# Performance work log

Measured on AMD Instinct MI355X. Metric: run time of the kernel, lower is better.

## Reference

```python
import jax, jax.numpy as jnp
import numpy as np


def _conv(x, w, b, pad):
    y = jax.lax.conv_general_dilated(
        x, w, window_strides=(1, 1), padding=[(pad, pad), (pad, pad)],
        dimension_numbers=('NCHW', 'OIHW', 'NCHW'))
    return y + b[None, :, None, None]


def _grid_sample(img, gxn, gyn):
    # img [N,C,H,W]; gxn,gyn [N,H,W] normalized coords.
    # Matches torch grid_sample(mode='bilinear', padding_mode='zeros', align_corners=False).
    N, C, H, W = img.shape
    ix = ((gxn + 1.0) * W - 1.0) * 0.5
    iy = ((gyn + 1.0) * H - 1.0) * 0.5
    ix0 = jnp.floor(ix); iy0 = jnp.floor(iy)
    ix1 = ix0 + 1.0; iy1 = iy0 + 1.0
    wx1 = ix - ix0; wy1 = iy - iy0
    wx0 = 1.0 - wx1; wy0 = 1.0 - wy1
    bidx = jnp.arange(N)[:, None, None]

    def gather(yy, xx):
        valid = (xx >= 0) & (xx < W) & (yy >= 0) & (yy < H)
        xc = jnp.clip(xx, 0, W - 1).astype(jnp.int32)
        yc = jnp.clip(yy, 0, H - 1).astype(jnp.int32)
        v = img[bidx, :, yc, xc]  # [N,H,W,C]
        return jnp.where(valid[..., None], v, jnp.zeros((), img.dtype))

    out = (gather(iy0, ix0) * (wy0 * wx0)[..., None]
           + gather(iy0, ix1) * (wy0 * wx1)[..., None]
           + gather(iy1, ix0) * (wy1 * wx0)[..., None]
           + gather(iy1, ix1) * (wy1 * wx1)[..., None])
    return jnp.transpose(out, (0, 3, 1, 2))  # [N,C,H,W]


def reference(inputs, state, i2h_w, i2h_b, i2f_w, i2f_b, h2f_w, h2f_b,
              flows_w, flows_b, wrap_w, wrap_b):
    B, T, Cin, H, W = inputs.shape
    hid = state.shape[1]
    L = flows_w.shape[0] // 2

    # input-to-hidden for all timesteps at once (as in the torch code)
    i2h = _conv(inputs.reshape(B * T, Cin, H, W), i2h_w, i2h_b, 1)
    i2h = i2h.reshape(B, T, 3 * hid, H, W)
    r_i, u_i, n_i = jnp.split(i2h, 3, axis=2)

    gx, gy = jnp.meshgrid(jnp.arange(W, dtype=inputs.dtype),
                          jnp.arange(H, dtype=inputs.dtype))  # each [H,W]

    def step(h, xs):
        x_t, r_t, u_t, n_t = xs
        f = jnp.tanh(_conv(x_t, i2f_w, i2f_b, 2) + _conv(h, h2f_w, h2f_b, 2))
        flows = _conv(f, flows_w, flows_b, 2).reshape(B, L, 2, H, W)
        # vgrid = grid + (-flow), then normalize by 2*v/size - 1
        vx = gx[None, None] - flows[:, :, 0]
        vy = gy[None, None] - flows[:, :, 1]
        gxn = 2.0 * vx / W - 1.0
        gyn = 2.0 * vy / H - 1.0
        img = jnp.broadcast_to(h[:, None], (B, L, hid, H, W)).reshape(B * L, hid, H, W)
        warped = _grid_sample(img, gxn.reshape(B * L, H, W), gyn.reshape(B * L, H, W))
        warped = warped.reshape(B, L * hid, H, W)
        h2h = _conv(warped, wrap_w, wrap_b, 0)
        r_h, u_h, n_h = jnp.split(h2h, 3, axis=1)
        r = jax.nn.sigmoid(r_t + r_h)
        u = jax.nn.sigmoid(u_t + u_h)
        n = jax.nn.sigmoid(n_t + r * n_h)  # note: sigmoid, faithful to source
        h_new = (1.0 - u) * n + u * h
        return h_new, h_new

    xs = (jnp.swapaxes(inputs, 0, 1),
          jnp.swapaxes(r_i, 0, 1),
          jnp.swapaxes(u_i, 0, 1),
          jnp.swapaxes(n_i, 0, 1))
    h_last, outs = jax.lax.scan(step, state, xs)
    outputs = jnp.swapaxes(outs, 0, 1)  # [B,T,hid,H,W]
    return outputs, h_last


def setup_inputs() -> dict:
    key = jax.random.key(0)
    ks = jax.random.split(key, 8)
    B, T, Cin, H, W = 4, 10, 8, 96, 96
    hid, L = 64, 13

    def w(k, shape):
        fan_in = int(np.prod(shape[1:]))
        return jax.random.normal(k, shape, jnp.float32) * (1.0 / np.sqrt(fan_in))

    return {
        'inputs': jax.random.normal(ks[0], (B, T, Cin, H, W), jnp.float32),
        'state': jnp.zeros((B, hid, H, W), jnp.float32),
        'i2h_w': w(ks[1], (3 * hid, Cin, 3, 3)), 'i2h_b': jnp.zeros((3 * hid,), jnp.float32),
        'i2f_w': w(ks[2], (32, Cin, 5, 5)), 'i2f_b': jnp.zeros((32,), jnp.float32),
        'h2f_w': w(ks[3], (32, hid, 5, 5)), 'h2f_b': jnp.zeros((32,), jnp.float32),
        'flows_w': w(ks[4], (2 * L, 32, 5, 5)), 'flows_b': jnp.zeros((2 * L,), jnp.float32),
        'wrap_w': w(ks[5], (3 * hid, hid * L, 1, 1)), 'wrap_b': jnp.zeros((3 * hid,), jnp.float32),
    }
```

## Files before the change

kernel.cpp:

```cpp
#include <hip/hip_runtime.h>
#include <math.h>

#define HW 9216

typedef __attribute__((ext_vector_type(8))) short short8;
typedef __attribute__((ext_vector_type(4))) short short4v;
typedef __attribute__((ext_vector_type(4))) float float4v;

__device__ __forceinline__ float sigmoidf_(float x) { return 1.0f / (1.0f + expf(-x)); }

__device__ __forceinline__ short bf16rne(float f) {
  unsigned u = __builtin_bit_cast(unsigned, f);
  unsigned r = (u + 0x7FFFu + ((u >> 16) & 1u)) >> 16;
  return (short)r;
}
__device__ __forceinline__ float bf2f(short s) {
  return __builtin_bit_cast(float, ((unsigned)(unsigned short)s) << 16);
}

__global__ __launch_bounds__(256) void k_wconv(const float* __restrict__ w,
                                               short* __restrict__ o)
{
  int i = blockIdx.x * 256 + threadIdx.x;
  if (i >= 192 * 832) return;
  int n = i / 832, k = i % 832;
  int l = k >> 6, c = k & 63;
  o[((size_t)l * 192 + n) * 64 + c] = bf16rne(w[i]);
}

__global__ __launch_bounds__(256) void k_pack(
    const float* __restrict__ wh, const float* __restrict__ wi,
    const float* __restrict__ flw, const float* __restrict__ wih,
    short* __restrict__ whK, short* __restrict__ wiK, short* __restrict__ flK,
    short* __restrict__ i2hK)
{
  int i = blockIdx.x * 256 + threadIdx.x;
  if (i < 51200) {
    int t = i / 2048, rem = i % 2048;
    int o = rem / 64, c = rem % 64;
    whK[i] = bf16rne(wh[((size_t)(o * 64 + c)) * 25 + t]);
  } else if (i < 58368) {
    int j = i - 51200;
    int g = j / 1024, rem = j % 1024;
    int o = rem / 32, k = rem % 32;
    int q = k / 8, ch = k % 8;
    int tap = g * 4 + q;
    wiK[j] = (tap < 25) ? bf16rne(wi[((size_t)(o * 8 + ch)) * 25 + tap]) : (short)0;
  } else if (i < 83968) {
    int j = i - 58368;
    int t = j / 1024, rem = j % 1024;
    int o = rem / 32, c = rem % 32;
    flK[j] = (o < 26) ? bf16rne(flw[((size_t)(o * 32 + c)) * 25 + t]) : (short)0;
  } else {
    int j = i - 83968;
    int g = j / 6144, rem = j % 6144;
    int n = rem / 32, k = rem % 32;
    int q = k / 8, ch = k % 8;
    int tap = g * 4 + q;
    i2hK[j] = (tap < 9) ? bf16rne(wih[((size_t)(n * 8 + ch)) * 9 + tap]) : (short)0;
  }
}

__global__ __launch_bounds__(256) void k_h2bf(const float* __restrict__ st,
                                              short* __restrict__ hbf)
{
  const int tid = threadIdx.x;
  const int pp = tid & 63, cg = tid >> 6;
  const int b = blockIdx.y;
  const int p = blockIdx.x * 64 + pp;
  short s[16];
  #pragma unroll
  for (int k = 0; k < 16; ++k)
    s[k] = bf16rne(st[((size_t)b * 64 + cg * 16 + k) * HW + p]);
  short* dst = hbf + ((size_t)b * HW + p) * 64 + cg * 16;
  *(short8*)dst = *(short8*)&s[0];
  *(short8*)(dst + 8) = *(short8*)&s[8];
}

__global__ __launch_bounds__(256) void k_x2bf(const float* __restrict__ inp,
                                              short* __restrict__ xbf)
{
  const int p  = blockIdx.x * 256 + threadIdx.x;
  const int bt = blockIdx.y;
  short s[8];
  #pragma unroll
  for (int ci = 0; ci < 8; ++ci)
    s[ci] = bf16rne(inp[((size_t)bt * 8 + ci) * HW + p]);
  *(short8*)(xbf + ((size_t)bt * HW + p) * 8) = *(short8*)s;
}

__global__ __launch_bounds__(256) void k_i2h(
    const short* __restrict__ xbf, int t_off,
    const short* __restrict__ wK, const float* __restrict__ bias,
    short* __restrict__ out)
{
  __shared__ __align__(16) short lds_o[192 * 136];
  const int tid  = threadIdx.x;
  const int lane = tid & 63;
  const int w    = tid >> 6;
  const int ml = lane & 15, qd = lane >> 4;
  const int zz = blockIdx.y;
  const int t = (zz >> 2) + t_off, b = zz & 3;
  const int pw0 = blockIdx.x * 128 + w * 32;
  const short* xb = xbf + ((size_t)(b * 10 + t)) * HW * 8;

  short8 afr[2][3];
  #pragma unroll
  for (int s = 0; s < 2; ++s) {
    int px0 = pw0 + s * 16;
    int y0 = px0 / 96, xc0 = px0 % 96;
    #pragma unroll
    for (int g = 0; g < 3; ++g) {
      int tap = g * 4 + qd;
      int dy = tap / 3 - 1;
      int dx = tap % 3 - 1;
      int yy = y0 + dy, xx = xc0 + ml + dx;
      bool v = (tap < 9) && (yy >= 0) && (yy < 96) && (xx >= 0) && (xx < 96);
      short8 a = {};
      if (v) a = *(const short8*)(xb + (size_t)(px0 + ml + dy * 96 + dx) * 8);
      afr[s][g] = a;
    }
  }

  float4v acc[2][12];
  #pragma unroll
  for (int s = 0; s < 2; ++s)
    #pragma unroll
    for (int j = 0; j < 12; ++j)
      #pragma unroll
      for (int r = 0; r < 4; ++r) acc[s][j][r] = 0.0f;

  #pragma unroll
  for (int j = 0; j < 12; ++j) {
    #pragma unroll
    for (int g = 0; g < 3; ++g) {
      short8 bf = *(const short8*)(wK + ((size_t)(g * 192 + j * 16 + ml)) * 32 + qd * 8);
      acc[0][j] = __builtin_amdgcn_mfma_f32_16x16x32_bf16(afr[0][g], bf, acc[0][j], 0, 0, 0);
      acc[1][j] = __builtin_amdgcn_mfma_f32_16x16x32_bf16(afr[1][g], bf, acc[1][j], 0, 0, 0);
    }
  }

  #pragma unroll
  for (int j = 0; j < 12; ++j) {
    float bv = bias[j * 16 + ml];
    #pragma unroll
    for (int s = 0; s < 2; ++s) {
      short4v o4;
      #pragma unroll
      for (int r = 0; r < 4; ++r) o4[r] = bf16rne(acc[s][j][r] + bv);
      *(short4v*)(lds_o + (j * 16 + ml) * 136 + w * 32 + s * 16 + qd * 4) = o4;
    }
  }
  __syncthreads();
  const int pblk = blockIdx.x * 128;
  #pragma unroll
  for (int k = 0; k < 12; ++k) {
    int r = (tid >> 4) + k * 16;
    short8 vvv = *(short8*)(lds_o + r * 136 + (tid & 15) * 8);
    *(short8*)(out + ((size_t)(zz * 192 + r)) * HW + pblk + (tid & 15) * 8) = vvv;
  }
}

__global__ __launch_bounds__(256) void k_f(
    const short* __restrict__ xbf, int t,
    const short* __restrict__ hbf,
    const short* __restrict__ whK,
    const short* __restrict__ wiK,
    const float* __restrict__ bi, const float* __restrict__ bh,
    short* __restrict__ fbf)
{
  const int tid = threadIdx.x;
  const int lane = tid & 63;
  const int w = tid >> 6;
  const int ml = lane & 15, qd = lane >> 4;
  const int b = blockIdx.y;
  const int px0 = blockIdx.x * 64 + w * 16;
  const int y0 = px0 / 96, xc0 = px0 % 96;
  const int xcol = xc0 + ml;
  const int px = px0 + ml;
  const short* hb = hbf + (size_t)b * HW * 64;
  const short* xb = xbf + ((size_t)(b * 10 + t)) * HW * 8;

  float4v acc0 = {0.f, 0.f, 0.f, 0.f};
  float4v acc1 = {0.f, 0.f, 0.f, 0.f};

  #pragma unroll
  for (int ky = 0; ky < 5; ++ky) {
    int yy = y0 + ky - 2;
    if (yy < 0 || yy >= 96) continue;
    #pragma unroll
    for (int kx = 0; kx < 5; ++kx) {
      int xx = xcol + kx - 2;
      bool cv = (xx >= 0) && (xx < 96);
      int off = (ky - 2) * 96 + (kx - 2);
      const short* ap = hb + (size_t)(px + off) * 64 + qd * 8;
      short8 a0 = {}, a1 = {};
      if (cv) { a0 = *(const short8*)ap; a1 = *(const short8*)(ap + 32); }
      int tap = ky * 5 + kx;
      const short* bp = whK + ((size_t)tap * 32 + ml) * 64 + qd * 8;
      short8 b00 = *(const short8*)bp;
      short8 b01 = *(const short8*)(bp + 32);
      short8 b10 = *(const short8*)(bp + 16 * 64);
      short8 b11 = *(const short8*)(bp + 16 * 64 + 32);
      acc0 = __builtin_amdgcn_mfma_f32_16x16x32_bf16(a0, b00, acc0, 0, 0, 0);
      acc0 = __builtin_amdgcn_mfma_f32_16x16x32_bf16(a1, b01, acc0, 0, 0, 0);
      acc1 = __builtin_amdgcn_mfma_f32_16x16x32_bf16(a0, b10, acc1, 0, 0, 0);
      acc1 = __builtin_amdgcn_mfma_f32_16x16x32_bf16(a1, b11, acc1, 0, 0, 0);
    }
  }

  #pragma unroll
  for (int g = 0; g < 7; ++g) {
    int tap = g * 4 + qd;
    int dy = tap / 5 - 2;
    int dx = tap - (dy + 2) * 5 - 2;
    int yy = y0 + dy, xx = xcol + dx;
    bool v = (tap < 25) && (yy >= 0) && (yy < 96) && (xx >= 0) && (xx < 96);
    short8 a = {};
    if (v) a = *(const short8*)(xb + (size_t)(px + dy * 96 + dx) * 8);
    const short* bp = wiK + ((size_t)g * 32 + ml) * 32 + qd * 8;
    short8 b0 = *(const short8*)bp;
    short8 b1 = *(const short8*)(bp + 16 * 32);
    acc0 = __builtin_amdgcn_mfma_f32_16x16x32_bf16(a, b0, acc0, 0, 0, 0);
    acc1 = __builtin_amdgcn_mfma_f32_16x16x32_bf16(a, b1, acc1, 0, 0, 0);
  }

  short* fo = fbf + (size_t)b * HW * 32;
  #pragma unroll
  for (int i = 0; i < 2; ++i) {
    int o = i * 16 + ml;
    float bias = bi[o] + bh[o];
    float4v a = i ? acc1 : acc0;
    #pragma unroll
    for (int r = 0; r < 4; ++r) {
      int p2 = px0 + qd * 4 + r;
      fo[(size_t)p2 * 32 + o] = bf16rne(tanhf(a[r] + bias));
    }
  }
}

__global__ __launch_bounds__(256) void k_flows(
    const short* __restrict__ fbf,
    const short* __restrict__ flK,
    const float* __restrict__ bias,
    float* __restrict__ fls)
{
  const int tid = threadIdx.x;
  const int lane = tid & 63;
  const int w = tid >> 6;
  const int ml = lane & 15, qd = lane >> 4;
  const int b = blockIdx.y;
  const int px0 = blockIdx.x * 64 + w * 16;
  const int y0 = px0 / 96, xc0 = px0 % 96;
  const int xcol = xc0 + ml;
  const int px = px0 + ml;
  const short* fb = fbf + (size_t)b * HW * 32;

  float4v acc0 = {0.f, 0.f, 0.f, 0.f};
  float4v acc1 = {0.f, 0.f, 0.f, 0.f};

  #pragma unroll
  for (int ky = 0; ky < 5; ++ky) {
    int yy = y0 + ky - 2;
    if (yy < 0 || yy >= 96) continue;
    #pragma unroll
    for (int kx = 0; kx < 5; ++kx) {
      int xx = xcol + kx - 2;
      bool cv = (xx >= 0) && (xx < 96);
      int off = (ky - 2) * 96 + (kx - 2);
      short8 a = {};
      if (cv) a = *(const short8*)(fb + (size_t)(px + off) * 32 + qd * 8);
      int tap = ky * 5 + kx;
      const short* bp = flK + ((size_t)tap * 32 + ml) * 32 + qd * 8;
      short8 b0 = *(const short8*)bp;
      short8 b1 = *(const short8*)(bp + 16 * 32);
      acc0 = __builtin_amdgcn_mfma_f32_16x16x32_bf16(a, b0, acc0, 0, 0, 0);
      acc1 = __builtin_amdgcn_mfma_f32_16x16x32_bf16(a, b1, acc1, 0, 0, 0);
    }
  }

  float* fo = fls + (size_t)b * 26 * HW;
  #pragma unroll
  for (int i = 0; i < 2; ++i) {
    int o = i * 16 + ml;
    if (o < 26) {
      float bv = bias[o];
      float4v a = i ? acc1 : acc0;
      #pragma unroll
      for (int r = 0; r < 4; ++r)
        fo[(size_t)o * HW + px0 + qd * 4 + r] = a[r] + bv;
    }
  }
}

__global__ __launch_bounds__(256, 3) void k_fused(
    const float* __restrict__ fls,
    const float* __restrict__ hbase, long long hstr,
    const short* __restrict__ hbf_in,
    const short* __restrict__ i2h,
    const short* __restrict__ wbf,
    const float* __restrict__ wb,
    float* __restrict__ outb, long long ostr,
    short* __restrict__ hbf_out,
    float* __restrict__ lastb)
{
  __shared__ __align__(16) char smem_raw[50176];
  short* lds_v0 = (short*)smem_raw;
  short* lds_v1 = lds_v0 + 64 * 80;
  float* lds_f  = (float*)(smem_raw + 20480);
  float* lds_h  = (float*)smem_raw;
  short* hpack  = (short*)smem_raw;

  const int tid = threadIdx.x;
  const int pp  = tid & 63;
  const int cg  = tid >> 6;
  const int ii  = blockIdx.x;
  const int xcd = ii & 7;
  const int b   = xcd >> 1;
  const int tile = ((ii >> 3) << 1) | (xcd & 1);
  const int p   = tile * 64 + pp;
  const int ypix = p / 96, xpix = p % 96;
  const float* hb  = hbase + (size_t)b * hstr;
  const short* hvp = hbf_in + ((size_t)b * HW) * 64 + cg * 16;
  const float* flb = fls + (size_t)b * 26 * HW;
  const int ml = pp & 15;
  const int qd = pp >> 4;
  const short* wfb = wbf + ((size_t)(48 * cg + ml)) * 64 + qd * 8;

  #pragma unroll
  for (int it = 0; it < 7; ++it) {
    int idx = it * 256 + tid;
    if (idx < 1664) {
      int c = idx >> 6, pp2 = idx & 63;
      lds_f[pp2 * 26 + c] = flb[(size_t)c * HW + tile * 64 + pp2];
    }
  }

  float4v acc[3][4];
  #pragma unroll
  for (int i = 0; i < 3; ++i)
    #pragma unroll
    for (int j = 0; j < 4; ++j)
      #pragma unroll
      for (int r = 0; r < 4; ++r) acc[i][j][r] = 0.0f;

  int   o_[4];
  float wt_[4];
  short8 u_[4][2];
  short8 wp[3][2];
  short vv[16];

  auto comp_offs = [&](int l) {
    float fx = lds_f[pp * 26 + 2 * l];
    float fy = lds_f[pp * 26 + 2 * l + 1];
    float ix = (float)xpix - fx - 0.5f;
    float iy = (float)ypix - fy - 0.5f;
    float x0f = floorf(ix), y0f = floorf(iy);
    float wx1 = ix - x0f, wy1 = iy - y0f;
    float wx0 = 1.0f - wx1, wy0 = 1.0f - wy1;
    int x0 = (int)x0f, y0 = (int)y0f;
    bool vx0 = (x0 >= 0) && (x0 < 96);
    bool vx1 = (x0 + 1 >= 0) && (x0 + 1 < 96);
    bool vy0g = (y0 >= 0) && (y0 < 96);
    bool vy1g = (y0 + 1 >= 0) && (y0 + 1 < 96);
    o_[0] = (vx0 && vy0g) ? (y0 * 96 + x0)           : -1;
    o_[1] = (vx1 && vy0g) ? (y0 * 96 + x0 + 1)       : -1;
    o_[2] = (vx0 && vy1g) ? ((y0 + 1) * 96 + x0)     : -1;
    o_[3] = (vx1 && vy1g) ? ((y0 + 1) * 96 + x0 + 1) : -1;
    wt_[0] = wy0 * wx0; wt_[1] = wy0 * wx1; wt_[2] = wy1 * wx0; wt_[3] = wy1 * wx1;
  };
  auto load_gather = [&]() {
    #pragma unroll
    for (int q = 0; q < 4; ++q) {
      short8 z = {};
      u_[q][0] = z; u_[q][1] = z;
      if (o_[q] >= 0) {
        const short* tp = hvp + (size_t)o_[q] * 64;
        u_[q][0] = *(const short8*)tp;
        u_[q][1] = *(const short8*)(tp + 8);
      }
    }
  };
  auto load_w = [&](int l) {
    const short* wsrc = wfb + (size_t)l * 192 * 64;
    #pragma unroll
    for (int i = 0; i < 3; ++i) {
      wp[i][0] = *(const short8*)(wsrc + (i * 16) * 64);
      wp[i][1] = *(const short8*)(wsrc + (i * 16) * 64 + 32);
    }
  };
  auto comp_vv = [&]() {
    float sum[16];
    #pragma unroll
    for (int k = 0; k < 16; ++k) sum[k] = 0.0f;
    #pragma unroll
    for (int q = 0; q < 4; ++q) {
      #pragma unroll
      for (int k = 0; k < 8; ++k) {
        sum[k]     += wt_[q] * bf2f(u_[q][0][k]);
        sum[k + 8] += wt_[q] * bf2f(u_[q][1][k]);
      }
    }
    #pragma unroll
    for (int k = 0; k < 16; ++k) vv[k] = bf16rne(sum[k]);
  };
  auto store_vv = [&](short* buf) {
    *(short8*)(buf + pp * 80 + cg * 16)     = *(short8*)&vv[0];
    *(short8*)(buf + pp * 80 + cg * 16 + 8) = *(short8*)&vv[8];
  };

  __syncthreads();
  comp_offs(0);
  load_gather();
  load_w(0);
  comp_vv();
  store_vv(lds_v0);

  for (int l = 0; l < 13; ++l) {
    __syncthreads();
    if (l < 12) {
      comp_offs(l + 1);
      load_gather();
    }
    short* rbuf = (l & 1) ? lds_v1 : lds_v0;
    #pragma unroll
    for (int ks = 0; ks < 2; ++ks) {
      short8 bfr[4];
      #pragma unroll
      for (int j = 0; j < 4; ++j)
        bfr[j] = *(const short8*)(rbuf + (j * 16 + ml) * 80 + ks * 32 + qd * 8);
      #pragma unroll
      for (int i = 0; i < 3; ++i)
        #pragma unroll
        for (int j = 0; j < 4; ++j)
          acc[i][j] = __builtin_amdgcn_mfma_f32_16x16x32_bf16(wp[i][ks], bfr[j], acc[i][j], 0, 0, 0);
    }
    if (l < 12) {
      load_w(l + 1);
      comp_vv();
      store_vv((l & 1) ? lds_v0 : lds_v1);
    }
  }

  __syncthreads();
  #pragma unroll
  for (int i = 0; i < 3; ++i)
    #pragma unroll
    for (int j = 0; j < 4; ++j)
      #pragma unroll
      for (int r = 0; r < 4; ++r) {
        int ch = 48 * cg + i * 16 + qd * 4 + r;
        int px = j * 16 + ml;
        lds_h[ch * 65 + px] = acc[i][j][r];
      }
  __syncthreads();

  const short* i2hb = i2h + (size_t)b * 192 * HW + p;
  float* ob = outb + (size_t)b * ostr;
  float hnv[16];
  #pragma unroll
  for (int k = 0; k < 16; ++k) {
    int cch = cg + k * 4;
    float rh = lds_h[cch * 65 + pp] + wb[cch];
    float uh = lds_h[(64 + cch) * 65 + pp] + wb[64 + cch];
    float nh = lds_h[(128 + cch) * 65 + pp] + wb[128 + cch];
    float rt = bf2f(i2hb[(size_t)cch * HW]);
    float ut = bf2f(i2hb[(size_t)(64 + cch) * HW]);
    float nt = bf2f(i2hb[(size_t)(128 + cch) * HW]);
    float rr = sigmoidf_(rt + rh);
    float uu = sigmoidf_(ut + uh);
    float nn = sigmoidf_(nt + rr * nh);
    float hp = hb[(size_t)cch * HW + p];
    float hn = (1.0f - uu) * nn + uu * hp;
    ob[(size_t)cch * HW + p] = hn;
    if (lastb) lastb[((size_t)b * 64 + cch) * HW + p] = hn;
    hnv[k] = hn;
  }

  __syncthreads();
  #pragma unroll
  for (int k = 0; k < 16; ++k)
    hpack[pp * 80 + cg + 4 * k] = bf16rne(hnv[k]);
  __syncthreads();
  {
    int px = tid >> 2, g = tid & 3;
    short8 a0 = *(short8*)(hpack + px * 80 + g * 16);
    short8 a1 = *(short8*)(hpack + px * 80 + g * 16 + 8);
    short* dst = hbf_out + ((size_t)b * HW + tile * 64 + px) * 64 + g * 16;
    *(short8*)dst = a0;
    *(short8*)(dst + 8) = a1;
  }
}

extern "C" void kernel_launch(void* const* d_in, const int* in_sizes, int n_in,
                              void* d_out, int out_size, void* d_ws, size_t ws_size,
                              hipStream_t stream)
{
  const float* inp   = (const float*)d_in[0];
  const float* state = (const float*)d_in[1];
  const float* i2h_w = (const float*)d_in[2];
  const float* i2h_b = (const float*)d_in[3];
  const float* i2f_w = (const float*)d_in[4];
  const float* i2f_b = (const float*)d_in[5];
  const float* h2f_w = (const float*)d_in[6];
  const float* h2f_b = (const float*)d_in[7];
  const float* fl_w  = (const float*)d_in[8];
  const float* fl_b  = (const float*)d_in[9];
  const float* wr_w  = (const float*)d_in[10];
  const float* wr_b  = (const float*)d_in[11];
  float* out = (float*)d_out;
  float* ws  = (float*)d_ws;

  const long long F_I2HB1 = 3538944;
  const long long F_FBF   = 589824;
  const long long F_FLS   = 958464;
  const long long F_HB    = 1179648;
  const long long F_XBF   = 1474560;
  const long long F_WBF   = 79872;
  const long long F_WHK   = 25600;
  const long long F_WIK   = 3584;
  const long long F_FLK   = 12800;
  const long long F_I2HK  = 9216;
  const long long OB      = (long long)10 * 64 * HW;

  const long long fixed = F_FBF + F_FLS + 2 * F_HB + F_XBF + F_WBF
                        + F_WHK + F_WIK + F_FLK + F_I2HK;
  bool batched = ws_size >= (size_t)(10 * F_I2HB1 + fixed) * 4ULL;
  long long i2h_fl = batched ? 10 * F_I2HB1 : F_I2HB1;

  short* ws_i2h = (short*)ws;
  float* fwp    = ws + i2h_fl;
  float* ws_fbf_f = fwp;              fwp += F_FBF;
  float* ws_fls   = fwp;              fwp += F_FLS;
  float* hbfA_f   = fwp;              fwp += F_HB;
  float* hbfB_f   = fwp;              fwp += F_HB;
  float* xbf_f    = fwp;              fwp += F_XBF;
  float* wbf_f    = fwp;              fwp += F_WBF;
  float* whK_f    = fwp;              fwp += F_WHK;
  float* wiK_f    = fwp;              fwp += F_WIK;
  float* flK_f    = fwp;              fwp += F_FLK;
  float* i2hK_f   = fwp;
  short* ws_fbf  = (short*)ws_fbf_f;
  short* hbfA    = (short*)hbfA_f;
  short* hbfB    = (short*)hbfB_f;
  short* ws_xbf  = (short*)xbf_f;
  short* ws_wbf  = (short*)wbf_f;
  short* ws_whK  = (short*)whK_f;
  short* ws_wiK  = (short*)wiK_f;
  short* ws_flK  = (short*)flK_f;
  short* ws_i2hK = (short*)i2hK_f;

  k_wconv<<<dim3(624), 256, 0, stream>>>(wr_w, ws_wbf);
  k_pack<<<dim3(400), 256, 0, stream>>>(h2f_w, i2f_w, fl_w, i2h_w,
                                        ws_whK, ws_wiK, ws_flK, ws_i2hK);
  k_h2bf<<<dim3(144, 4), 256, 0, stream>>>(state, hbfA);
  k_x2bf<<<dim3(36, 40), 256, 0, stream>>>(inp, ws_xbf);
  if (batched)
    k_i2h<<<dim3(72, 40), 256, 0, stream>>>(ws_xbf, 0, ws_i2hK, i2h_b, ws_i2h);

  for (int t = 0; t < 10; ++t) {
    const float* hbase = (t == 0) ? state : (out + (size_t)(t - 1) * 64 * HW);
    long long hstr = (t == 0) ? (long long)64 * HW : OB;
    short* hin  = (t & 1) ? hbfB : hbfA;
    short* hout = (t & 1) ? hbfA : hbfB;

    if (!batched)
      k_i2h<<<dim3(72, 4), 256, 0, stream>>>(ws_xbf, t, ws_i2hK, i2h_b, ws_i2h);
    k_f<<<dim3(144, 4), 256, 0, stream>>>(ws_xbf, t, hin, ws_whK, ws_wiK,
                                          i2f_b, h2f_b, ws_fbf);
    k_flows<<<dim3(144, 4), 256, 0, stream>>>(ws_fbf, ws_flK, fl_b, ws_fls);

    const short* i2h_t = batched ? (ws_i2h + (size_t)t * 2 * F_I2HB1) : ws_i2h;
    float* outbase = out + (size_t)t * 64 * HW;
    float* lastb = (t == 9) ? (out + (size_t)4 * 10 * 64 * HW) : nullptr;
    k_fused<<<dim3(576), 256, 0, stream>>>(ws_fls, hbase, hstr, hin, i2h_t,
                                           ws_wbf, wr_b, outbase, OB, hout, lastb);
  }
}
```

Before: 1.621 ms.

## Remap MFMA channel ownership so gate epilogue runs from registers, shrink LDS

Each wave's output channels are remapped so it holds matching r/u/n channels (ch, 64+ch, 128+ch). This lets the GRU gate epilogue read accumulators straight from registers instead of transposing through a large LDS staging buffer. The double-buffered sampled-value LDS is replaced by a single buffer with an extra barrier per flow level. Total LDS drops from about 49 KB to about 15.5 KB, and launch bounds rise to 4 blocks per CU. In exchange it adds a sync per iteration, and the epilogue global accesses become less coalesced (16-pixel runs per channel).

```diff
diff --git a/kernel.cpp b/kernel.cpp
--- a/kernel.cpp
+++ b/kernel.cpp
@@ -293,7 +293,7 @@
   }
 }
 
-__global__ __launch_bounds__(256, 3) void k_fused(
+__global__ __launch_bounds__(256, 4) void k_fused(
     const float* __restrict__ fls,
     const float* __restrict__ hbase, long long hstr,
     const short* __restrict__ hbf_in,
@@ -304,12 +304,10 @@
     short* __restrict__ hbf_out,
     float* __restrict__ lastb)
 {
-  __shared__ __align__(16) char smem_raw[50176];
-  short* lds_v0 = (short*)smem_raw;
-  short* lds_v1 = lds_v0 + 64 * 80;
-  float* lds_f  = (float*)(smem_raw + 20480);
-  float* lds_h  = (float*)smem_raw;
-  short* hpack  = (short*)smem_raw;
+  __shared__ __align__(16) char smem_raw[15872];
+  short* lds_v = (short*)smem_raw;
+  float* lds_f = (float*)(smem_raw + 9216);
+  short* hpack = (short*)smem_raw;
 
   const int tid = threadIdx.x;
   const int pp  = tid & 63;
@@ -325,7 +323,7 @@
   const float* flb = fls + (size_t)b * 26 * HW;
   const int ml = pp & 15;
   const int qd = pp >> 4;
-  const short* wfb = wbf + ((size_t)(48 * cg + ml)) * 64 + qd * 8;
+  const short* wfb = wbf + ((size_t)(cg * 16 + ml)) * 64 + qd * 8;
 
   #pragma unroll
   for (int it = 0; it < 7; ++it) {
@@ -385,8 +383,8 @@
     const short* wsrc = wfb + (size_t)l * 192 * 64;
     #pragma unroll
     for (int i = 0; i < 3; ++i) {
-      wp[i][0] = *(const short8*)(wsrc + (i * 16) * 64);
-      wp[i][1] = *(const short8*)(wsrc + (i * 16) * 64 + 32);
+      wp[i][0] = *(const short8*)(wsrc + (size_t)(i * 64) * 64);
+      wp[i][1] = *(const short8*)(wsrc + (size_t)(i * 64) * 64 + 32);
     }
   };
   auto comp_vv = [&]() {
@@ -404,31 +402,28 @@
     #pragma unroll
     for (int k = 0; k < 16; ++k) vv[k] = bf16rne(sum[k]);
   };
-  auto store_vv = [&](short* buf) {
-    *(short8*)(buf + pp * 80 + cg * 16)     = *(short8*)&vv[0];
-    *(short8*)(buf + pp * 80 + cg * 16 + 8) = *(short8*)&vv[8];
-  };
 
   __syncthreads();
+  load_w(0);
   comp_offs(0);
   load_gather();
-  load_w(0);
   comp_vv();
-  store_vv(lds_v0);
 
   for (int l = 0; l < 13; ++l) {
+    __syncthreads();
+    *(short8*)(lds_v + pp * 72 + cg * 16)     = *(short8*)&vv[0];
+    *(short8*)(lds_v + pp * 72 + cg * 16 + 8) = *(short8*)&vv[8];
     __syncthreads();
     if (l < 12) {
       comp_offs(l + 1);
       load_gather();
     }
-    short* rbuf = (l & 1) ? lds_v1 : lds_v0;
     #pragma unroll
     for (int ks = 0; ks < 2; ++ks) {
       short8 bfr[4];
       #pragma unroll
       for (int j = 0; j < 4; ++j)
-        bfr[j] = *(const short8*)(rbuf + (j * 16 + ml) * 80 + ks * 32 + qd * 8);
+        bfr[j] = *(const short8*)(lds_v + (j * 16 + ml) * 72 + ks * 32 + qd * 8);
       #pragma unroll
       for (int i = 0; i < 3; ++i)
         #pragma unroll
@@ -438,54 +433,42 @@
     if (l < 12) {
       load_w(l + 1);
       comp_vv();
-      store_vv((l & 1) ? lds_v0 : lds_v1);
     }
   }
 
   __syncthreads();
-  #pragma unroll
-  for (int i = 0; i < 3; ++i)
-    #pragma unroll
-    for (int j = 0; j < 4; ++j)
-      #pragma unroll
-      for (int r = 0; r < 4; ++r) {
-        int ch = 48 * cg + i * 16 + qd * 4 + r;
-        int px = j * 16 + ml;
-        lds_h[ch * 65 + px] = acc[i][j][r];
-      }
-  __syncthreads();
-
-  const short* i2hb = i2h + (size_t)b * 192 * HW + p;
+  const short* i2hb = i2h + (size_t)b * 192 * HW;
   float* ob = outb + (size_t)b * ostr;
-  float hnv[16];
-  #pragma unroll
-  for (int k = 0; k < 16; ++k) {
-    int cch = cg + k * 4;
-    float rh = lds_h[cch * 65 + pp] + wb[cch];
-    float uh = lds_h[(64 + cch) * 65 + pp] + wb[64 + cch];
-    float nh = lds_h[(128 + cch) * 65 + pp] + wb[128 + cch];
-    float rt = bf2f(i2hb[(size_t)cch * HW]);
-    float ut = bf2f(i2hb[(size_t)(64 + cch) * HW]);
-    float nt = bf2f(i2hb[(size_t)(128 + cch) * HW]);
-    float rr = sigmoidf_(rt + rh);
-    float uu = sigmoidf_(ut + uh);
-    float nn = sigmoidf_(nt + rr * nh);
-    float hp = hb[(size_t)cch * HW + p];
-    float hn = (1.0f - uu) * nn + uu * hp;
-    ob[(size_t)cch * HW + p] = hn;
-    if (lastb) lastb[((size_t)b * 64 + cch) * HW + p] = hn;
-    hnv[k] = hn;
-  }
-
-  __syncthreads();
-  #pragma unroll
-  for (int k = 0; k < 16; ++k)
-    hpack[pp * 80 + cg + 4 * k] = bf16rne(hnv[k]);
+  const int chb = cg * 16 + qd * 4;
+  #pragma unroll
+  for (int j = 0; j < 4; ++j) {
+    const int pe = tile * 64 + j * 16 + ml;
+    short4v s4;
+    #pragma unroll
+    for (int r = 0; r < 4; ++r) {
+      int ch = chb + r;
+      float rh = acc[0][j][r] + wb[ch];
+      float uh = acc[1][j][r] + wb[64 + ch];
+      float nh = acc[2][j][r] + wb[128 + ch];
+      float rt = bf2f(i2hb[(size_t)ch * HW + pe]);
+      float ut = bf2f(i2hb[(size_t)(64 + ch) * HW + pe]);
+      float nt = bf2f(i2hb[(size_t)(128 + ch) * HW + pe]);
+      float rr = sigmoidf_(rt + rh);
+      float uu = sigmoidf_(ut + uh);
+      float nn = sigmoidf_(nt + rr * nh);
+      float hp = hb[(size_t)ch * HW + pe];
+      float hn = (1.0f - uu) * nn + uu * hp;
+      ob[(size_t)ch * HW + pe] = hn;
+      if (lastb) lastb[((size_t)b * 64 + ch) * HW + pe] = hn;
+      s4[r] = bf16rne(hn);
+    }
+    *(short4v*)(hpack + (j * 16 + ml) * 72 + chb) = s4;
+  }
   __syncthreads();
   {
     int px = tid >> 2, g = tid & 3;
-    short8 a0 = *(short8*)(hpack + px * 80 + g * 16);
-    short8 a1 = *(short8*)(hpack + px * 80 + g * 16 + 8);
+    short8 a0 = *(short8*)(hpack + px * 72 + g * 16);
+    short8 a1 = *(short8*)(hpack + px * 72 + g * 16 + 8);
     short* dst = hbf_out + ((size_t)b * HW + tile * 64 + px) * 64 + g * 16;
     *(short8*)dst = a0;
     *(short8*)(dst + 8) = a1;
```

After: 1.892 ms. +16.7%, slower.
